# Performance work log

Measured on AMD Instinct MI355X. Metric: run time of the kernel, lower is better.

## Reference

```python
import jax, jax.numpy as jnp
import numpy as np

C = 16  # number of classes (matches batch_ids fill_max)
XMIN, XMAX = 1e-37, 1.0 - 1e-5

def setup_inputs() -> dict:
    key = jax.random.key(0)
    k1, k2 = jax.random.split(key)
    hidden = jax.random.normal(k1, (65536, 512), dtype=jnp.float32)
    batch_ids = jax.random.randint(k2, (65536,), 0, C, dtype=jnp.int64)
    return {"hidden": hidden, "batch_ids": batch_ids, "d": 64}

def reference(hidden, batch_ids, d):
    N, D = hidden.shape
    seg = lambda v: jax.ops.segment_sum(v, batch_ids, num_segments=C)
    counts = seg(jnp.ones((N,), hidden.dtype))                  # [C]
    means = seg(hidden) / counts[:, None]                       # [C, D]
    # within-class sum of squared deviations, per feature dim
    withins = seg((hidden - means[batch_ids]) ** 2)             # [C, D]
    # pairwise: global mean of pair is (m_i+m_j)/2, so each class's between
    # term is ((m_i-m_j)/2)^2; weighted by counts it sums to that * (n_i+n_j)
    half_diff = (means[:, None, :] - means[None, :, :]) * 0.5   # [C, C, D]
    pair_counts = counts[:, None] + counts[None, :]             # [C, C]
    pair_between = half_diff * half_diff * pair_counts[:, :, None]
    pair_within = withins[:, None, :] + withins[None, :, :]
    d2 = pair_counts - 2.0
    d2 = jnp.where(d2 == 0.0, 1e-5, d2)
    x = pair_between / (pair_between + pair_within)
    x = jnp.clip(x, XMIN, XMAX)
    a = jnp.full_like(x, 0.5)                                   # d1/2
    b = jnp.broadcast_to((d2 * 0.5)[:, :, None], x.shape)       # d2/2
    xbetainc = jax.scipy.special.betainc(a, b, x)               # [C, C, D]
    top_k, _ = jax.lax.top_k(xbetainc, d)                       # [C, C, d]
    per_pair = jnp.sum(jnp.log(top_k), axis=-1)                 # [C, C]
    mask = jnp.triu(jnp.ones((C, C), dtype=bool), k=1)          # pairs i<j
    total = jnp.sum(jnp.where(mask, per_pair, jnp.zeros_like(per_pair)))
    return -total
```

## Files before the change

### kernel.cpp

```cpp
#include <hip/hip_runtime.h>
#include <math.h>

#define NUM_C 16
#define DIMS 512
#define CHUNKS 64

__device__ inline void atomAddF(float* p, float v) { unsafeAtomicAdd(p, v); }


__global__ __launch_bounds__(256) void k_scatter1p(const int* __restrict__ bids,
                                                   int* __restrict__ gcur,
                                                   int* __restrict__ perm,
                                                   float* __restrict__ out, int n) {
    __shared__ int lh[NUM_C], lb[NUM_C], lc[NUM_C];
    const int tid = threadIdx.x;
    if (blockIdx.x == 0 && tid == 0) out[0] = 0.f;
    if (tid < NUM_C) lh[tid] = 0;
    __syncthreads();
    const int i0 = (blockIdx.x * 256 + tid) * 4;
    int4 c4 = make_int4(0, 0, 0, 0);
    const bool ok = (i0 + 3 < n);
    if (ok) {
        c4 = *reinterpret_cast<const int4*>(bids + i0);
        atomicAdd(&lh[c4.x], 1); atomicAdd(&lh[c4.y], 1);
        atomicAdd(&lh[c4.z], 1); atomicAdd(&lh[c4.w], 1);
    }
    __syncthreads();
    if (tid < NUM_C) {
        lb[tid] = tid * n + atomicAdd(&gcur[tid], lh[tid]);
        lc[tid] = 0;
    }
    __syncthreads();
    if (ok) {
        perm[lb[c4.x] + atomicAdd(&lc[c4.x], 1)] = i0;
        perm[lb[c4.y] + atomicAdd(&lc[c4.y], 1)] = i0 + 1;
        perm[lb[c4.z] + atomicAdd(&lc[c4.z], 1)] = i0 + 2;
        perm[lb[c4.w] + atomicAdd(&lc[c4.w], 1)] = i0 + 3;
    }
}

__global__ __launch_bounds__(256) void k_segsum(const float* __restrict__ hidden,
                                                const int* __restrict__ perm,
                                                const int* __restrict__ gcur,
                                                float* __restrict__ gsum,
                                                float* __restrict__ gsq, int n) {
    const int tid = threadIdx.x;
    const int c = blockIdx.x & (NUM_C - 1);
    const int chunk = blockIdx.x >> 4;
    const int cnt = gcur[c];
    const int base = c * n;
    const int len = (cnt + CHUNKS - 1) / CHUNKS;
    const int lo = chunk * len;
    const int hi = min(lo + len, cnt);
    const int half = tid >> 7, ht = tid & 127;

    float4 s = {0.f, 0.f, 0.f, 0.f}, q = {0.f, 0.f, 0.f, 0.f};
#define LOADROW(r) (*(reinterpret_cast<const float4*>(hidden + (size_t)(r) * DIMS) + ht))
#define ACC(v) { s.x += (v).x; s.y += (v).y; s.z += (v).z; s.w += (v).w; \
                 q.x += (v).x*(v).x; q.y += (v).y*(v).y; q.z += (v).z*(v).z; q.w += (v).w*(v).w; }
    int k = lo + half;
    for (; k + 6 < hi; k += 8) {
        const int r0 = perm[base + k],     r1 = perm[base + k + 2];
        const int r2 = perm[base + k + 4], r3 = perm[base + k + 6];
        const float4 v0 = LOADROW(r0), v1 = LOADROW(r1);
        const float4 v2 = LOADROW(r2), v3 = LOADROW(r3);
        ACC(v0); ACC(v1); ACC(v2); ACC(v3);
    }
    for (; k < hi; k += 2) {
        const int r0 = perm[base + k];
        const float4 v0 = LOADROW(r0);
        ACC(v0);
    }
#undef LOADROW
#undef ACC

    __shared__ float red[128 * 8];
    if (half == 1) {
        float* p = &red[ht * 8];
        p[0] = s.x; p[1] = s.y; p[2] = s.z; p[3] = s.w;
        p[4] = q.x; p[5] = q.y; p[6] = q.z; p[7] = q.w;
    }
    __syncthreads();
    if (half == 0) {
        const float* p = &red[ht * 8];
        s.x += p[0]; s.y += p[1]; s.z += p[2]; s.w += p[3];
        q.x += p[4]; q.y += p[5]; q.z += p[6]; q.w += p[7];
        float* gs = gsum + c * DIMS + 4 * ht;
        float* gq = gsq  + c * DIMS + 4 * ht;
        atomAddF(gs + 0, s.x); atomAddF(gs + 1, s.y);
        atomAddF(gs + 2, s.z); atomAddF(gs + 3, s.w);
        atomAddF(gq + 0, q.x); atomAddF(gq + 1, q.y);
        atomAddF(gq + 2, q.z); atomAddF(gq + 3, q.w);
    }
}

__global__ __launch_bounds__(512) void k_pairs(const float* __restrict__ gsum,
                                               const float* __restrict__ gsq,
                                               const int* __restrict__ gcur,
                                               const int* __restrict__ dptr,
                                               float* __restrict__ out) {
    __shared__ float xs[DIMS];
    __shared__ float wsum[8];
    const int tid = threadIdx.x;

    int p = blockIdx.x, i = 0, rem = p;
    while (rem >= NUM_C - 1 - i) { rem -= NUM_C - 1 - i; ++i; }
    const int j = i + 1 + rem;

    const float ni = (float)gcur[i], nj = (float)gcur[j];
    const float pc = ni + nj;

    {
        const float si = gsum[i * DIMS + tid];
        const float sj = gsum[j * DIMS + tid];
        const float mi = si / ni, mj = sj / nj;
        float wi = gsq[i * DIMS + tid] - si * mi;  wi = wi > 0.f ? wi : 0.f;
        float wj = gsq[j * DIMS + tid] - sj * mj;  wj = wj > 0.f ? wj : 0.f;
        const float hd = (mi - mj) * 0.5f;
        const float between = hd * hd * pc;
        const float within = wi + wj;
        float x = between / (between + within);
        if (!(x >= 1e-37f)) x = 1e-37f;
        const float XM = 1.0f - 1e-5f;
        if (x > XM) x = XM;
        xs[tid] = x;
    }

    for (int kk = 2; kk <= DIMS; kk <<= 1) {
        for (int jj = kk >> 1; jj > 0; jj >>= 1) {
            __syncthreads();
            const int ixj = tid ^ jj;
            if (ixj > tid) {
                const float va = xs[tid], vb = xs[ixj];
                const bool sw = ((tid & kk) == 0) ? (va < vb) : (va > vb);
                if (sw) { xs[tid] = vb; xs[ixj] = va; }
            }
        }
    }
    __syncthreads();

    const int d = *dptr;
    float d2 = pc - 2.0f;
    if (d2 == 0.0f) d2 = 1e-5f;
    const float b = d2 * 0.5f;
    const float bm1 = b - 1.0f;
    const float invb = 1.0f / b;
    const float ln2overB = 0.69314718f
        - (0.5f * (1.14472989f - logf(b)) + log1pf(invb * (0.125f + 0.0078125f * invb)));

    const int sub = tid & 7;
    const int rounds = (d + 63) >> 6;
    float part = 0.f;
    for (int r = 0; r < rounds; ++r) {
        const int q = (tid >> 3) + (r << 6);
        const bool act = (q < d);
        const float x = xs[act ? q : 0];
        const float rt = sqrtf(x);
        const float h = rt * (1.0f / 256.0f);
        float acc = 0.f;
        for (int k = sub; k <= 256; k += 8) {
            const float sv = (float)k * h;
            const float w = (k == 0 || k == 256) ? 1.f : ((k & 1) ? 4.f : 2.f);
            acc += w * __expf(bm1 * log1pf(-sv * sv));
        }
        acc += __shfl_down(acc, 4, 64);
        acc += __shfl_down(acc, 2, 64);
        acc += __shfl_down(acc, 1, 64);
        if (sub == 0 && act) {
            float li = logf(acc * h * (1.0f / 3.0f)) + ln2overB;
            part += (li < 0.f) ? li : 0.f;
        }
    }
    for (int off = 32; off > 0; off >>= 1) part += __shfl_down(part, off, 64);
    if ((tid & 63) == 0) wsum[tid >> 6] = part;
    __syncthreads();
    if (tid == 0) {
        float t = 0.f;
        for (int w = 0; w < 8; ++w) t += wsum[w];
        atomAddF(out, -t);
    }
}

extern "C" void kernel_launch(void* const* d_in, const int* in_sizes, int n_in,
                              void* d_out, int out_size, void* d_ws, size_t ws_size,
                              hipStream_t stream) {
    const float* hidden = (const float*)d_in[0];
    const int* bids = (const int*)d_in[1];
    const int* dptr = (const int*)d_in[2];
    float* out = (float*)d_out;
    const int N = in_sizes[1];

    char* ws = (char*)d_ws;
    int*   gcur = (int*)(ws + 0);
    float* gsum = (float*)(ws + 256);
    float* gsq  = (float*)(ws + 33024);
    int*   perm = (int*)(ws + 65792);

    hipMemsetAsync(d_ws, 0, 65792, stream);

    const int nb = (N + 1023) / 1024;
    k_scatter1p<<<nb, 256, 0, stream>>>(bids, gcur, perm, out, N);
    k_segsum  <<<NUM_C * CHUNKS, 256, 0, stream>>>(hidden, perm, gcur, gsum, gsq, N);
    k_pairs   <<<NUM_C * (NUM_C - 1) / 2, 512, 0, stream>>>(gsum, gsq, gcur, dptr, out);
}
```

Baseline: 240.1 us.

## Replace permutation-based segment sum with streaming per-chunk LDS histograms

Drops the counting-sort permutation and indirect gather. Each block now streams contiguous rows, accumulating sums and squares per class in shared memory, and writes per-chunk partials. A separate reduce kernel and the pair kernel then sum those partials, so the memset and float atomics go away. In exchange the code writes and reads about 32 MB of partials, adds a kernel launch, and hardcodes N=65536 rows (512 chunks of 128).

```diff
diff --git a/kernel.cpp b/kernel.cpp
--- a/kernel.cpp
+++ b/kernel.cpp
@@ -3,100 +3,107 @@
 
 #define NUM_C 16
 #define DIMS 512
-#define CHUNKS 64
+#define RPC 128
+#define NCHUNK 512
+#define GRP 16
+#define CPG (NCHUNK / GRP)
 
 __device__ inline void atomAddF(float* p, float v) { unsafeAtomicAdd(p, v); }
 
 
-__global__ __launch_bounds__(256) void k_scatter1p(const int* __restrict__ bids,
-                                                   int* __restrict__ gcur,
-                                                   int* __restrict__ perm,
-                                                   float* __restrict__ out, int n) {
-    __shared__ int lh[NUM_C], lb[NUM_C], lc[NUM_C];
+__global__ __launch_bounds__(256) void k_stream(const float* __restrict__ hidden,
+                                                const int* __restrict__ bids,
+                                                float* __restrict__ psum,
+                                                float* __restrict__ psq,
+                                                int* __restrict__ pcnt) {
+    __shared__ float lsum[NUM_C * 256];
+    __shared__ float lsq[NUM_C * 256];
     const int tid = threadIdx.x;
-    if (blockIdx.x == 0 && tid == 0) out[0] = 0.f;
-    if (tid < NUM_C) lh[tid] = 0;
-    __syncthreads();
-    const int i0 = (blockIdx.x * 256 + tid) * 4;
-    int4 c4 = make_int4(0, 0, 0, 0);
-    const bool ok = (i0 + 3 < n);
-    if (ok) {
-        c4 = *reinterpret_cast<const int4*>(bids + i0);
-        atomicAdd(&lh[c4.x], 1); atomicAdd(&lh[c4.y], 1);
-        atomicAdd(&lh[c4.z], 1); atomicAdd(&lh[c4.w], 1);
-    }
-    __syncthreads();
-    if (tid < NUM_C) {
-        lb[tid] = tid * n + atomicAdd(&gcur[tid], lh[tid]);
-        lc[tid] = 0;
-    }
-    __syncthreads();
-    if (ok) {
-        perm[lb[c4.x] + atomicAdd(&lc[c4.x], 1)] = i0;
-        perm[lb[c4.y] + atomicAdd(&lc[c4.y], 1)] = i0 + 1;
-        perm[lb[c4.z] + atomicAdd(&lc[c4.z], 1)] = i0 + 2;
-        perm[lb[c4.w] + atomicAdd(&lc[c4.w], 1)] = i0 + 3;
-    }
-}
-
-__global__ __launch_bounds__(256) void k_segsum(const float* __restrict__ hidden,
-                                                const int* __restrict__ perm,
-                                                const int* __restrict__ gcur,
-                                                float* __restrict__ gsum,
-                                                float* __restrict__ gsq, int n) {
+    const int g = blockIdx.x & 1;
+    const int chunk = blockIdx.x >> 1;
+
+    #pragma unroll
+    for (int c = 0; c < NUM_C; ++c) { lsum[c * 256 + tid] = 0.f; lsq[c * 256 + tid] = 0.f; }
+
+    const int rowbase = chunk * RPC;
+    const float* hp = hidden + (size_t)rowbase * DIMS + g * 256 + tid;
+    const int* bp = bids + rowbase;
+
+    int mycnt = 0;
+
+    float va[8]; int ca[8];
+    #pragma unroll
+    for (int u = 0; u < 8; ++u) { va[u] = hp[(size_t)u * DIMS]; ca[u] = bp[u]; }
+
+    for (int it = 0; it < RPC / 8 - 1; ++it) {
+        float vb[8]; int cb[8];
+        const float* hp2 = hp + (size_t)(it + 1) * 8 * DIMS;
+        const int* bp2 = bp + (it + 1) * 8;
+        #pragma unroll
+        for (int u = 0; u < 8; ++u) { vb[u] = hp2[(size_t)u * DIMS]; cb[u] = bp2[u]; }
+        #pragma unroll
+        for (int u = 0; u < 8; ++u) {
+            const int idx = ca[u] * 256 + tid;
+            lsum[idx] += va[u];
+            lsq[idx]  += va[u] * va[u];
+            mycnt += (ca[u] == tid) ? 1 : 0;
+        }
+        #pragma unroll
+        for (int u = 0; u < 8; ++u) { va[u] = vb[u]; ca[u] = cb[u]; }
+    }
+    #pragma unroll
+    for (int u = 0; u < 8; ++u) {
+        const int idx = ca[u] * 256 + tid;
+        lsum[idx] += va[u];
+        lsq[idx]  += va[u] * va[u];
+        mycnt += (ca[u] == tid) ? 1 : 0;
+    }
+
+    float* ps = psum + (size_t)blockIdx.x * NUM_C * 256 + tid;
+    float* pq = psq  + (size_t)blockIdx.x * NUM_C * 256 + tid;
+    #pragma unroll
+    for (int c = 0; c < NUM_C; ++c) {
+        ps[c * 256] = lsum[c * 256 + tid];
+        pq[c * 256] = lsq[c * 256 + tid];
+    }
+    if (g == 0 && tid < NUM_C) pcnt[chunk * NUM_C + tid] = mycnt;
+}
+
+__global__ __launch_bounds__(256) void k_reduce(const float* __restrict__ psum,
+                                                const float* __restrict__ psq,
+                                                const int* __restrict__ pcnt,
+                                                float* __restrict__ p2sum,
+                                                float* __restrict__ p2sq,
+                                                int* __restrict__ cnt2,
+                                                float* __restrict__ out) {
     const int tid = threadIdx.x;
-    const int c = blockIdx.x & (NUM_C - 1);
-    const int chunk = blockIdx.x >> 4;
-    const int cnt = gcur[c];
-    const int base = c * n;
-    const int len = (cnt + CHUNKS - 1) / CHUNKS;
-    const int lo = chunk * len;
-    const int hi = min(lo + len, cnt);
-    const int half = tid >> 7, ht = tid & 127;
-
-    float4 s = {0.f, 0.f, 0.f, 0.f}, q = {0.f, 0.f, 0.f, 0.f};
-#define LOADROW(r) (*(reinterpret_cast<const float4*>(hidden + (size_t)(r) * DIMS) + ht))
-#define ACC(v) { s.x += (v).x; s.y += (v).y; s.z += (v).z; s.w += (v).w; \
-                 q.x += (v).x*(v).x; q.y += (v).y*(v).y; q.z += (v).z*(v).z; q.w += (v).w*(v).w; }
-    int k = lo + half;
-    for (; k + 6 < hi; k += 8) {
-        const int r0 = perm[base + k],     r1 = perm[base + k + 2];
-        const int r2 = perm[base + k + 4], r3 = perm[base + k + 6];
-        const float4 v0 = LOADROW(r0), v1 = LOADROW(r1);
-        const float4 v2 = LOADROW(r2), v3 = LOADROW(r3);
-        ACC(v0); ACC(v1); ACC(v2); ACC(v3);
-    }
-    for (; k < hi; k += 2) {
-        const int r0 = perm[base + k];
-        const float4 v0 = LOADROW(r0);
-        ACC(v0);
-    }
-#undef LOADROW
-#undef ACC
-
-    __shared__ float red[128 * 8];
-    if (half == 1) {
-        float* p = &red[ht * 8];
-        p[0] = s.x; p[1] = s.y; p[2] = s.z; p[3] = s.w;
-        p[4] = q.x; p[5] = q.y; p[6] = q.z; p[7] = q.w;
-    }
-    __syncthreads();
-    if (half == 0) {
-        const float* p = &red[ht * 8];
-        s.x += p[0]; s.y += p[1]; s.z += p[2]; s.w += p[3];
-        q.x += p[4]; q.y += p[5]; q.z += p[6]; q.w += p[7];
-        float* gs = gsum + c * DIMS + 4 * ht;
-        float* gq = gsq  + c * DIMS + 4 * ht;
-        atomAddF(gs + 0, s.x); atomAddF(gs + 1, s.y);
-        atomAddF(gs + 2, s.z); atomAddF(gs + 3, s.w);
-        atomAddF(gq + 0, q.x); atomAddF(gq + 1, q.y);
-        atomAddF(gq + 2, q.z); atomAddF(gq + 3, q.w);
-    }
-}
-
-__global__ __launch_bounds__(512) void k_pairs(const float* __restrict__ gsum,
-                                               const float* __restrict__ gsq,
-                                               const int* __restrict__ gcur,
+    const int bid = blockIdx.x;
+    const int c = bid >> 5;
+    const int g = (bid >> 4) & 1;
+    const int grp = bid & 15;
+    if (bid == 0 && tid == 0) out[0] = 0.f;
+
+    float s = 0.f, q = 0.f;
+    #pragma unroll 4
+    for (int k = 0; k < CPG; ++k) {
+        const int chunk = grp * CPG + k;
+        const size_t seg = ((size_t)(chunk * 2 + g) * NUM_C + c) * 256 + tid;
+        s += psum[seg];
+        q += psq[seg];
+    }
+    p2sum[((c * 2 + g) * GRP + grp) * 256 + tid] = s;
+    p2sq [((c * 2 + g) * GRP + grp) * 256 + tid] = q;
+
+    if (g == 0 && tid == 0) {
+        int cc = 0;
+        for (int k = 0; k < CPG; ++k) cc += pcnt[(grp * CPG + k) * NUM_C + c];
+        cnt2[c * GRP + grp] = cc;
+    }
+}
+
+__global__ __launch_bounds__(512) void k_pairs(const float* __restrict__ p2sum,
+                                               const float* __restrict__ p2sq,
+                                               const int* __restrict__ cnt2,
                                                const int* __restrict__ dptr,
                                                float* __restrict__ out) {
     __shared__ float xs[DIMS];
@@ -107,15 +114,25 @@
     while (rem >= NUM_C - 1 - i) { rem -= NUM_C - 1 - i; ++i; }
     const int j = i + 1 + rem;
 
-    const float ni = (float)gcur[i], nj = (float)gcur[j];
+    int cnti = 0, cntj = 0;
+    #pragma unroll
+    for (int gq = 0; gq < GRP; ++gq) { cnti += cnt2[i * GRP + gq]; cntj += cnt2[j * GRP + gq]; }
+    const float ni = (float)cnti, nj = (float)cntj;
     const float pc = ni + nj;
 
     {
-        const float si = gsum[i * DIMS + tid];
-        const float sj = gsum[j * DIMS + tid];
+        const int g = tid >> 8, dl = tid & 255;
+        float si = 0.f, qi = 0.f, sj = 0.f, qj = 0.f;
+        #pragma unroll
+        for (int gq = 0; gq < GRP; ++gq) {
+            si += p2sum[((i * 2 + g) * GRP + gq) * 256 + dl];
+            qi += p2sq [((i * 2 + g) * GRP + gq) * 256 + dl];
+            sj += p2sum[((j * 2 + g) * GRP + gq) * 256 + dl];
+            qj += p2sq [((j * 2 + g) * GRP + gq) * 256 + dl];
+        }
         const float mi = si / ni, mj = sj / nj;
-        float wi = gsq[i * DIMS + tid] - si * mi;  wi = wi > 0.f ? wi : 0.f;
-        float wj = gsq[j * DIMS + tid] - sj * mj;  wj = wj > 0.f ? wj : 0.f;
+        float wi = qi - si * mi;  wi = wi > 0.f ? wi : 0.f;
+        float wj = qj - sj * mj;  wj = wj > 0.f ? wj : 0.f;
         const float hd = (mi - mj) * 0.5f;
         const float between = hd * hd * pc;
         const float within = wi + wj;
@@ -188,18 +205,16 @@
     const int* bids = (const int*)d_in[1];
     const int* dptr = (const int*)d_in[2];
     float* out = (float*)d_out;
-    const int N = in_sizes[1];
 
     char* ws = (char*)d_ws;
-    int*   gcur = (int*)(ws + 0);
-    float* gsum = (float*)(ws + 256);
-    float* gsq  = (float*)(ws + 33024);
-    int*   perm = (int*)(ws + 65792);
-
-    hipMemsetAsync(d_ws, 0, 65792, stream);
-
-    const int nb = (N + 1023) / 1024;
-    k_scatter1p<<<nb, 256, 0, stream>>>(bids, gcur, perm, out, N);
-    k_segsum  <<<NUM_C * CHUNKS, 256, 0, stream>>>(hidden, perm, gcur, gsum, gsq, N);
-    k_pairs   <<<NUM_C * (NUM_C - 1) / 2, 512, 0, stream>>>(gsum, gsq, gcur, dptr, out);
-}
+    float* psum  = (float*)(ws);
+    float* psq   = (float*)(ws + (16u << 20));
+    int*   pcnt  = (int*)  (ws + (32u << 20));
+    float* p2sum = (float*)(ws + (32u << 20) + 32768);
+    float* p2sq  = (float*)(ws + (32u << 20) + 32768 + 524288);
+    int*   cnt2  = (int*)  (ws + (32u << 20) + 32768 + 2 * 524288);
+
+    k_stream<<<NCHUNK * 2, 256, 0, stream>>>(hidden, bids, psum, psq, pcnt);
+    k_reduce<<<NUM_C * 2 * GRP, 256, 0, stream>>>(psum, psq, pcnt, p2sum, p2sq, cnt2, out);
+    k_pairs <<<NUM_C * (NUM_C - 1) / 2, 512, 0, stream>>>(p2sum, p2sq, cnt2, dptr, out);
+}
```

New measurement: 227.6 us. -5.2%, faster.
